# Performance work log

Measured on AMD Instinct MI355X. Metric: run time of the kernel, lower is better.

## Reference

```python
import jax, jax.numpy as jnp
import numpy as np
import math

N, DM, DK, DV, KWIN = 500, 2048, 2048, 2048, 10

def _xavier(key, shape):
    fan_out, fan_in = shape[0], shape[1]
    limit = math.sqrt(6.0 / (fan_in + fan_out))
    return jax.random.uniform(key, (shape[0], shape[1]), jnp.float32, -limit, limit)

def setup_inputs() -> dict:
    key = jax.random.key(0)
    ks = jax.random.split(key, 7)
    X = jax.random.normal(ks[0], (N, DM), jnp.float32)
    mask = jax.random.randint(ks[1], (N, N), 0, 2, jnp.int32)
    # torch Linear weight is (out, in); store transposed so fwd is X @ W
    Wq = _xavier(ks[2], (DK, DM)).T  # [DM, DK]
    Wk = _xavier(ks[3], (DK, DM)).T
    Wv = _xavier(ks[4], (DV, DM)).T
    Wo = _xavier(ks[5], (DM, DV)).T  # [DV, DM]
    wk = _xavier(ks[6], (2 * KWIN + 1, DM))  # relative-position embedding table
    return {"X": X, "mask": mask, "Wq": Wq, "Wk": Wk, "Wv": Wv, "Wo": Wo, "wk": wk}

def reference(X, mask, Wq, Wk, Wv, Wo, wk):
    n = X.shape[0]
    scale = 1.0 / math.sqrt(DK)
    Q = X @ Wq            # [n, dk]
    K = X @ Wk            # [n, dk]
    V = X @ Wv            # [n, dv]
    Qs = Q * scale
    S = Qs @ K.T          # [n, n] content scores
    # relative-position bias: Sr[i,j] = Qs[i] . wk[clip(j-i,-k,k)+k]
    # (Shaw-style gather; identical math to wk[table] matmul, no [n,n,dm] intermediate)
    idx = jnp.clip(jnp.arange(n)[None, :] - jnp.arange(n)[:, None], -KWIN, KWIN) + KWIN  # [n, n]
    QR = Qs @ wk.T                                   # [n, 2k+1]
    Sr = jnp.take_along_axis(QR, idx, axis=1)        # [n, n]
    S = S + Sr
    S = jnp.where(mask == 0, jnp.float32(-1e9), S)
    A = jax.nn.softmax(S, axis=-1)                   # dropout_rate=0 -> identity
    Y = (A @ V) @ Wo                                 # [n, dm]
    return (Y, A)
```

## Files before the change

### kernel.cpp

```cpp
#include <hip/hip_runtime.h>
#include <hip/hip_bf16.h>


#define N_TOK 500
#define MP 512
#define DM 2048
#define KWIN_ 10
#define NREL 21

typedef __hip_bfloat16 bf16;
typedef __attribute__((ext_vector_type(8))) short short8;
typedef __attribute__((ext_vector_type(4))) float floatx4;

#define NS 262144L

__device__ inline float bfj(const short8& v, int j) {
  return __bfloat162float(((const bf16*)&v)[j]);
}

__device__ __forceinline__ void transpose_tile(const float* __restrict__ W,
                                               bf16* __restrict__ Out, int k0,
                                               int n0) {
  __shared__ float t[64][68];
  int tid = threadIdx.x;
  int rr = tid >> 4, cc = (tid & 15) * 4;
  int gsw = cc >> 2;
#pragma unroll
  for (int p = 0; p < 4; ++p) {
    int r = rr + 16 * p;
    float4 v = *(const float4*)(W + (long)(k0 + r) * DM + n0 + cc);
    *(float4*)&t[r][(gsw ^ (r & 3)) * 4] = v;
  }
  __syncthreads();
#pragma unroll
  for (int s0 = 0; s0 < 2; ++s0) {
    int s = tid + s0 * 256;
    int n = s >> 3, c = s & 7;
    bf16 v[8];
#pragma unroll
    for (int j = 0; j < 8; ++j) {
      int rowt = c * 8 + j;
      int col = ((n >> 2) ^ (rowt & 3)) * 4 + (n & 3);
      v[j] = __float2bfloat16(t[rowt][col]);
    }
    *(short8*)(Out + (long)(n0 + n) * DM + k0 + c * 8) = *(short8*)v;
  }
}

__global__ __launch_bounds__(256) void prep(
    const float* __restrict__ Wq, const float* __restrict__ Wk,
    const float* __restrict__ Wv, const float* __restrict__ X,
    const float* __restrict__ wk, bf16* __restrict__ WqkT,
    bf16* __restrict__ WvT, bf16* __restrict__ Xb, bf16* __restrict__ wkb) {
  int z = blockIdx.z;
  int tid = threadIdx.x;
  if (z == 3) {
    int row = blockIdx.y * 32 + blockIdx.x;
    int c0 = tid * 8;
    bf16 v[8];
    if (row < MP) {
      if (row < N_TOK) {
        const float* p = X + (long)row * DM + c0;
#pragma unroll
        for (int j = 0; j < 8; ++j) v[j] = __float2bfloat16(p[j]);
      } else {
#pragma unroll
        for (int j = 0; j < 8; ++j) v[j] = __float2bfloat16(0.f);
      }
      *(short8*)(Xb + (long)row * DM + c0) = *(short8*)v;
    } else if (row < MP + NREL) {
      int r = row - MP;
      const float* p = wk + (long)r * DM + c0;
#pragma unroll
      for (int j = 0; j < 8; ++j) v[j] = __float2bfloat16(p[j]);
      *(short8*)(wkb + (long)r * DM + c0) = *(short8*)v;
    }
    return;
  }
  const float* W = (z == 0) ? Wq : (z == 1) ? Wk : Wv;
  bf16* Out = (z == 0) ? WqkT : (z == 1) ? (WqkT + (long)DM * DM) : WvT;
  transpose_tile(W, Out, blockIdx.y * 64, blockIdx.x * 64);
}

template <int OUT>
__device__ __forceinline__ void gemm_core(
    const bf16* __restrict__ A, int lda, const bf16* __restrict__ B, int ldb,
    float* __restrict__ Cf, bf16* __restrict__ Cb, int ldc, int kStart,
    int kLen, int row0, int col0, int m_store) {
  __shared__ __align__(16) bf16 As[128][32];
  __shared__ __align__(16) bf16 Bs[128][32];
  int tid = threadIdx.x;
  int lane = tid & 63, w = tid >> 6;
  int wr = (w & 1) * 64, wc = (w >> 1) * 64;
  int l16 = lane & 15, l4 = lane >> 4;
  int r1 = tid >> 2, c1 = (tid & 3) * 8;
  const bf16* Ab = A + (long)row0 * lda + kStart;
  const bf16* Bb = B + (long)col0 * ldb + kStart;
  const bf16* a1p = Ab + (long)r1 * lda + c1;
  const bf16* a2p = Ab + (long)(r1 + 64) * lda + c1;
  const bf16* b1p = Bb + (long)r1 * ldb + c1;
  const bf16* b2p = Bb + (long)(r1 + 64) * ldb + c1;
  floatx4 acc[4][4] = {};
  short8 pa0 = *(const short8*)a1p, pa1 = *(const short8*)a2p;
  short8 pb0 = *(const short8*)b1p, pb1 = *(const short8*)b2p;
  for (int k0 = 0; k0 < kLen; k0 += 32) {
    if (k0) __syncthreads();
    *(short8*)&As[r1][c1] = pa0;
    *(short8*)&As[r1 + 64][c1] = pa1;
    *(short8*)&Bs[r1][c1] = pb0;
    *(short8*)&Bs[r1 + 64][c1] = pb1;
    __syncthreads();
    int kn = k0 + 32;
    if (kn < kLen) {
      pa0 = *(const short8*)(a1p + kn);
      pa1 = *(const short8*)(a2p + kn);
      pb0 = *(const short8*)(b1p + kn);
      pb1 = *(const short8*)(b2p + kn);
    }
    short8 af[4], bg[4];
#pragma unroll
    for (int g = 0; g < 4; ++g)
      af[g] = *(short8*)&As[wr + g * 16 + l16][l4 * 8];
#pragma unroll
    for (int g = 0; g < 4; ++g)
      bg[g] = *(short8*)&Bs[wc + g * 16 + l16][l4 * 8];
#pragma unroll
    for (int g = 0; g < 4; ++g)
#pragma unroll
      for (int h = 0; h < 4; ++h)
        acc[g][h] =
            __builtin_amdgcn_mfma_f32_16x16x32_bf16(af[g], bg[h], acc[g][h], 0, 0, 0);
  }
#pragma unroll
  for (int g = 0; g < 4; ++g)
#pragma unroll
    for (int h = 0; h < 4; ++h)
#pragma unroll
      for (int i = 0; i < 4; ++i) {
        long r = row0 + wr + g * 16 + l4 * 4 + i;
        long c = col0 + wc + h * 16 + l16;
        if (OUT == 0)
          Cf[r * ldc + c] = acc[g][h][i];
        else if (OUT == 1)
          Cb[r * ldc + c] = __float2bfloat16(acc[g][h][i]);
        else {
          if (r < m_store) atomicAdd(&Cf[r * ldc + c], acc[g][h][i]);
        }
      }
}

__global__ __launch_bounds__(256, 2) void gemm_qkvt(
    const bf16* __restrict__ Xb, const bf16* __restrict__ WqkT,
    const bf16* __restrict__ WvT, bf16* __restrict__ QKbf,
    bf16* __restrict__ Vtb) {
  int id = blockIdx.x;
  if (id < 128) {
    int col0 = (id & 31) * 128, row0 = (id >> 5) * 128;
    gemm_core<1>(Xb, DM, WqkT, DM, nullptr, QKbf, 4096, 0, DM, row0, col0, 0);
  } else {
    int t = id - 128;
    int col0 = (t & 3) * 128, row0 = (t >> 2) * 128;
    gemm_core<1>(WvT, DM, Xb, DM, nullptr, Vtb, MP, 0, DM, row0, col0, 0);
  }
}

__global__ __launch_bounds__(256, 2) void gemm_s(const bf16* __restrict__ QKbf,
                                                 float* __restrict__ Sp) {
  gemm_core<0>(QKbf, 4096, QKbf + 2048, 4096, Sp + (long)blockIdx.z * NS,
               nullptr, MP, blockIdx.z * 512, 512, blockIdx.y * 128,
               blockIdx.x * 128, 0);
}

__global__ __launch_bounds__(256, 2) void gemm_av_wot(
    const bf16* __restrict__ Abf, const bf16* __restrict__ Vtb,
    bf16* __restrict__ AVbf, const float* __restrict__ Wo,
    bf16* __restrict__ WoT) {
  int id = blockIdx.x;
  if (id < 64) {
    int col0 = (id & 15) * 128, row0 = (id >> 4) * 128;
    gemm_core<1>(Abf, MP, Vtb, MP, nullptr, AVbf, DM, 0, MP, row0, col0, 0);
  } else {
    int t = id - 64;
    transpose_tile(Wo, WoT, (t >> 5) * 64, (t & 31) * 64);
  }
}

__global__ __launch_bounds__(256, 2) void gemm_y(const bf16* __restrict__ AVbf,
                                                 const bf16* __restrict__ WoT,
                                                 float* __restrict__ Yout) {
  gemm_core<2>(AVbf, DM, WoT, DM, Yout, nullptr, DM, blockIdx.z * 1024, 1024,
               blockIdx.y * 128, blockIdx.x * 128, N_TOK);
}

__global__ __launch_bounds__(256) void softmax_qr(
    const float* __restrict__ Sp, const bf16* __restrict__ QKbf,
    const bf16* __restrict__ wkb, const int* __restrict__ mask,
    float* __restrict__ Aout, bf16* __restrict__ Abf,
    float* __restrict__ Yout) {
  int i = blockIdx.x;
  int tid = threadIdx.x;
  if (i >= N_TOK) {
    Abf[(long)i * MP + tid] = __float2bfloat16(0.f);
    Abf[(long)i * MP + tid + 256] = __float2bfloat16(0.f);
    return;
  }
  {
    float4 z4 = {0.f, 0.f, 0.f, 0.f};
    float* yr = Yout + (long)i * DM + tid * 8;
    *(float4*)yr = z4;
    *(float4*)(yr + 4) = z4;
  }
  int lane = tid & 63, w = tid >> 6;
  __shared__ float sQR[24];
  __shared__ float red[4];
  short8 q[4];
#pragma unroll
  for (int s = 0; s < 4; ++s)
    q[s] = *(const short8*)(QKbf + (long)i * 4096 + s * 512 + lane * 8);
  for (int r = w; r < NREL; r += 4) {
    float p = 0.f;
#pragma unroll
    for (int s = 0; s < 4; ++s) {
      short8 wv = *(const short8*)(wkb + (long)r * DM + s * 512 + lane * 8);
#pragma unroll
      for (int j = 0; j < 8; ++j) p += bfj(q[s], j) * bfj(wv, j);
    }
#pragma unroll
    for (int o = 32; o > 0; o >>= 1) p += __shfl_down(p, o);
    if (lane == 0) sQR[r] = p;
  }
  __syncthreads();
  const float scale = 0.022097086912079608f;
  float v0, v1 = -1e30f;
  int j0 = tid, j1 = tid + 256;
  {
    float s = Sp[(long)i * MP + j0] + Sp[NS + (long)i * MP + j0] +
              Sp[2 * NS + (long)i * MP + j0] + Sp[3 * NS + (long)i * MP + j0];
    int rel = j0 - i;
    rel = rel < -KWIN_ ? -KWIN_ : (rel > KWIN_ ? KWIN_ : rel);
    s = scale * (s + sQR[rel + KWIN_]);
    if (mask[(long)i * N_TOK + j0] == 0) s = -1e9f;
    v0 = s;
  }
  if (j1 < N_TOK) {
    float s = Sp[(long)i * MP + j1] + Sp[NS + (long)i * MP + j1] +
              Sp[2 * NS + (long)i * MP + j1] + Sp[3 * NS + (long)i * MP + j1];
    int rel = j1 - i;
    rel = rel < -KWIN_ ? -KWIN_ : (rel > KWIN_ ? KWIN_ : rel);
    s = scale * (s + sQR[rel + KWIN_]);
    if (mask[(long)i * N_TOK + j1] == 0) s = -1e9f;
    v1 = s;
  }
  float mx = fmaxf(v0, v1);
#pragma unroll
  for (int o = 32; o > 0; o >>= 1) mx = fmaxf(mx, __shfl_down(mx, o));
  if (lane == 0) red[w] = mx;
  __syncthreads();
  if (tid == 0) red[0] = fmaxf(fmaxf(red[0], red[1]), fmaxf(red[2], red[3]));
  __syncthreads();
  mx = red[0];
  __syncthreads();
  float e0 = expf(v0 - mx);
  float e1 = (j1 < N_TOK) ? expf(v1 - mx) : 0.f;
  float sum = e0 + e1;
#pragma unroll
  for (int o = 32; o > 0; o >>= 1) sum += __shfl_down(sum, o);
  if (lane == 0) red[w] = sum;
  __syncthreads();
  if (tid == 0) red[0] = red[0] + red[1] + red[2] + red[3];
  __syncthreads();
  float inv = 1.f / red[0];
  float a0 = e0 * inv, a1 = e1 * inv;
  Aout[(long)i * N_TOK + j0] = a0;
  if (j1 < N_TOK) Aout[(long)i * N_TOK + j1] = a1;
  Abf[(long)i * MP + j0] = __float2bfloat16(a0);
  Abf[(long)i * MP + j1] = __float2bfloat16(a1);
}

extern "C" void kernel_launch(void* const* d_in, const int* in_sizes, int n_in,
                              void* d_out, int out_size, void* d_ws,
                              size_t ws_size, hipStream_t stream) {
  const float* X = (const float*)d_in[0];
  const int* mask = (const int*)d_in[1];
  const float* Wq = (const float*)d_in[2];
  const float* Wk = (const float*)d_in[3];
  const float* Wv = (const float*)d_in[4];
  const float* Wo = (const float*)d_in[5];
  const float* wk = (const float*)d_in[6];

  float* Yout = (float*)d_out;
  float* Aout = Yout + (long)N_TOK * DM;

  const long MB = 1 << 20;
  char* p = (char*)d_ws;
  bf16* Xb = (bf16*)p;
  bf16* WqkT = (bf16*)(p + 2 * MB);
  bf16* WvT = (bf16*)(p + 18 * MB);
  bf16* WoT = (bf16*)(p + 26 * MB);
  bf16* wkb = (bf16*)(p + 34 * MB);
  bf16* QKbf = (bf16*)(p + 35 * MB);
  bf16* Vtb = (bf16*)(p + 39 * MB);
  float* Sp = (float*)(p + 41 * MB);
  bf16* Abf = (bf16*)(p + 45 * MB);
  bf16* AVbf = (bf16*)(p + 46 * MB);

  dim3 b256(256);

  prep<<<dim3(32, 32, 4), b256, 0, stream>>>(Wq, Wk, Wv, X, wk, WqkT, WvT, Xb,
                                             wkb);
  gemm_qkvt<<<dim3(192), b256, 0, stream>>>(Xb, WqkT, WvT, QKbf, Vtb);
  gemm_s<<<dim3(4, 4, 4), b256, 0, stream>>>(QKbf, Sp);
  softmax_qr<<<dim3(MP), b256, 0, stream>>>(Sp, QKbf, wkb, mask, Aout, Abf,
                                            Yout);
  gemm_av_wot<<<dim3(1088), b256, 0, stream>>>(Abf, Vtb, AVbf, Wo, WoT);
  gemm_y<<<dim3(16, 4, 2), b256, 0, stream>>>(AVbf, WoT, Yout);
}
```

Baseline: 196.8 us.

## Fuse all stages into one persistent kernel with software grid barriers

Replaces the six separate kernel launches with a single persistent kernel of 256 blocks that runs every stage and separates them with an atomic-counter grid barrier. It also computes Q, K and V in one GEMM and transposes V afterwards, splits the S GEMM into eight K-slices instead of four, and double-buffers the GEMM shared-memory tiles. The aim is to remove launch gaps and raise parallelism. In exchange, the grid barriers require all 256 blocks to be co-resident, and several phases leave most blocks idle.

```diff
diff --git a/kernel.cpp b/kernel.cpp
--- a/kernel.cpp
+++ b/kernel.cpp
@@ -7,6 +7,7 @@
 #define DM 2048
 #define KWIN_ 10
 #define NREL 21
+#define NB 256
 
 typedef __hip_bfloat16 bf16;
 typedef __attribute__((ext_vector_type(8))) short short8;
@@ -18,10 +19,23 @@
   return __bfloat162float(((const bf16*)&v)[j]);
 }
 
+__device__ __forceinline__ void gsync(int* bar, int it) {
+  __syncthreads();
+  if (threadIdx.x == 0) {
+    __threadfence();
+    atomicAdd(bar, 1);
+    while (__hip_atomic_load(bar, __ATOMIC_ACQUIRE,
+                             __HIP_MEMORY_SCOPE_AGENT) < NB * it)
+      __builtin_amdgcn_s_sleep(1);
+  }
+  __syncthreads();
+  __threadfence();
+}
+
 __device__ __forceinline__ void transpose_tile(const float* __restrict__ W,
                                                bf16* __restrict__ Out, int k0,
-                                               int n0) {
-  __shared__ float t[64][68];
+                                               int n0, char* sm) {
+  float (*t)[68] = (float(*)[68])sm;
   int tid = threadIdx.x;
   int rr = tid >> 4, cc = (tid & 15) * 4;
   int gsw = cc >> 2;
@@ -45,91 +59,93 @@
     }
     *(short8*)(Out + (long)(n0 + n) * DM + k0 + c * 8) = *(short8*)v;
   }
-}
-
-__global__ __launch_bounds__(256) void prep(
-    const float* __restrict__ Wq, const float* __restrict__ Wk,
-    const float* __restrict__ Wv, const float* __restrict__ X,
-    const float* __restrict__ wk, bf16* __restrict__ WqkT,
-    bf16* __restrict__ WvT, bf16* __restrict__ Xb, bf16* __restrict__ wkb) {
-  int z = blockIdx.z;
-  int tid = threadIdx.x;
-  if (z == 3) {
-    int row = blockIdx.y * 32 + blockIdx.x;
-    int c0 = tid * 8;
-    bf16 v[8];
-    if (row < MP) {
-      if (row < N_TOK) {
-        const float* p = X + (long)row * DM + c0;
-#pragma unroll
-        for (int j = 0; j < 8; ++j) v[j] = __float2bfloat16(p[j]);
-      } else {
-#pragma unroll
-        for (int j = 0; j < 8; ++j) v[j] = __float2bfloat16(0.f);
-      }
-      *(short8*)(Xb + (long)row * DM + c0) = *(short8*)v;
-    } else if (row < MP + NREL) {
-      int r = row - MP;
-      const float* p = wk + (long)r * DM + c0;
-#pragma unroll
-      for (int j = 0; j < 8; ++j) v[j] = __float2bfloat16(p[j]);
-      *(short8*)(wkb + (long)r * DM + c0) = *(short8*)v;
-    }
-    return;
-  }
-  const float* W = (z == 0) ? Wq : (z == 1) ? Wk : Wv;
-  bf16* Out = (z == 0) ? WqkT : (z == 1) ? (WqkT + (long)DM * DM) : WvT;
-  transpose_tile(W, Out, blockIdx.y * 64, blockIdx.x * 64);
+  __syncthreads();
+}
+
+__device__ __forceinline__ void transpose_bf(const bf16* __restrict__ src,
+                                             int lds, bf16* __restrict__ dst,
+                                             int ldd, int r0, int c0,
+                                             char* sm) {
+  unsigned short (*t)[72] = (unsigned short(*)[72])sm;
+  const unsigned short* s = (const unsigned short*)src;
+  unsigned short* d = (unsigned short*)dst;
+  int tid = threadIdx.x;
+  int c = tid & 63, r4 = tid >> 6;
+#pragma unroll
+  for (int i = 0; i < 16; ++i) {
+    int r = r4 * 16 + i;
+    t[r][c] = s[(long)(r0 + r) * lds + c0 + c];
+  }
+  __syncthreads();
+#pragma unroll
+  for (int i = 0; i < 16; ++i) {
+    int r = r4 * 16 + i;
+    d[(long)(c0 + r) * ldd + r0 + c] = t[c][r];
+  }
+  __syncthreads();
 }
 
 template <int OUT>
 __device__ __forceinline__ void gemm_core(
     const bf16* __restrict__ A, int lda, const bf16* __restrict__ B, int ldb,
     float* __restrict__ Cf, bf16* __restrict__ Cb, int ldc, int kStart,
-    int kLen, int row0, int col0, int m_store) {
-  __shared__ __align__(16) bf16 As[128][32];
-  __shared__ __align__(16) bf16 Bs[128][32];
+    int kLen, int row0, int col0, int m_store, char* sm) {
+  bf16* As = (bf16*)sm;
+  bf16* Bs = (bf16*)(sm + 16384);
   int tid = threadIdx.x;
   int lane = tid & 63, w = tid >> 6;
   int wr = (w & 1) * 64, wc = (w >> 1) * 64;
   int l16 = lane & 15, l4 = lane >> 4;
   int r1 = tid >> 2, c1 = (tid & 3) * 8;
-  const bf16* Ab = A + (long)row0 * lda + kStart;
-  const bf16* Bb = B + (long)col0 * ldb + kStart;
-  const bf16* a1p = Ab + (long)r1 * lda + c1;
-  const bf16* a2p = Ab + (long)(r1 + 64) * lda + c1;
-  const bf16* b1p = Bb + (long)r1 * ldb + c1;
-  const bf16* b2p = Bb + (long)(r1 + 64) * ldb + c1;
+  int soff = r1 * 32 + c1;
+  const bf16* a1p = A + (long)(row0 + r1) * lda + kStart + c1;
+  const bf16* a2p = a1p + 64 * (long)lda;
+  const bf16* b1p = B + (long)(col0 + r1) * ldb + kStart + c1;
+  const bf16* b2p = b1p + 64 * (long)ldb;
   floatx4 acc[4][4] = {};
   short8 pa0 = *(const short8*)a1p, pa1 = *(const short8*)a2p;
   short8 pb0 = *(const short8*)b1p, pb1 = *(const short8*)b2p;
+  *(short8*)(As + soff) = pa0;
+  *(short8*)(As + 2048 + soff) = pa1;
+  *(short8*)(Bs + soff) = pb0;
+  *(short8*)(Bs + 2048 + soff) = pb1;
+  if (kLen > 32) {
+    pa0 = *(const short8*)(a1p + 32);
+    pa1 = *(const short8*)(a2p + 32);
+    pb0 = *(const short8*)(b1p + 32);
+    pb1 = *(const short8*)(b2p + 32);
+  }
+  __syncthreads();
+  int cur = 0;
   for (int k0 = 0; k0 < kLen; k0 += 32) {
-    if (k0) __syncthreads();
-    *(short8*)&As[r1][c1] = pa0;
-    *(short8*)&As[r1 + 64][c1] = pa1;
-    *(short8*)&Bs[r1][c1] = pb0;
-    *(short8*)&Bs[r1 + 64][c1] = pb1;
-    __syncthreads();
-    int kn = k0 + 32;
-    if (kn < kLen) {
-      pa0 = *(const short8*)(a1p + kn);
-      pa1 = *(const short8*)(a2p + kn);
-      pb0 = *(const short8*)(b1p + kn);
-      pb1 = *(const short8*)(b2p + kn);
-    }
+    int cb = cur * 4096, nb = (cur ^ 1) * 4096;
     short8 af[4], bg[4];
 #pragma unroll
     for (int g = 0; g < 4; ++g)
-      af[g] = *(short8*)&As[wr + g * 16 + l16][l4 * 8];
+      af[g] = *(short8*)(As + cb + (wr + g * 16 + l16) * 32 + l4 * 8);
 #pragma unroll
     for (int g = 0; g < 4; ++g)
-      bg[g] = *(short8*)&Bs[wc + g * 16 + l16][l4 * 8];
+      bg[g] = *(short8*)(Bs + cb + (wc + g * 16 + l16) * 32 + l4 * 8);
+    if (k0 + 32 < kLen) {
+      *(short8*)(As + nb + soff) = pa0;
+      *(short8*)(As + nb + 2048 + soff) = pa1;
+      *(short8*)(Bs + nb + soff) = pb0;
+      *(short8*)(Bs + nb + 2048 + soff) = pb1;
+      if (k0 + 64 < kLen) {
+        pa0 = *(const short8*)(a1p + k0 + 64);
+        pa1 = *(const short8*)(a2p + k0 + 64);
+        pb0 = *(const short8*)(b1p + k0 + 64);
+        pb1 = *(const short8*)(b2p + k0 + 64);
+      }
+    }
 #pragma unroll
     for (int g = 0; g < 4; ++g)
 #pragma unroll
       for (int h = 0; h < 4; ++h)
         acc[g][h] =
             __builtin_amdgcn_mfma_f32_16x16x32_bf16(af[g], bg[h], acc[g][h], 0, 0, 0);
+    __syncthreads();
+    cur ^= 1;
   }
 #pragma unroll
   for (int g = 0; g < 4; ++g)
@@ -143,80 +159,28 @@
           Cf[r * ldc + c] = acc[g][h][i];
         else if (OUT == 1)
           Cb[r * ldc + c] = __float2bfloat16(acc[g][h][i]);
-        else {
-          if (r < m_store) atomicAdd(&Cf[r * ldc + c], acc[g][h][i]);
-        }
+        else if (r < m_store)
+          atomicAdd(&Cf[r * ldc + c], acc[g][h][i]);
       }
 }
 
-__global__ __launch_bounds__(256, 2) void gemm_qkvt(
-    const bf16* __restrict__ Xb, const bf16* __restrict__ WqkT,
-    const bf16* __restrict__ WvT, bf16* __restrict__ QKbf,
-    bf16* __restrict__ Vtb) {
-  int id = blockIdx.x;
-  if (id < 128) {
-    int col0 = (id & 31) * 128, row0 = (id >> 5) * 128;
-    gemm_core<1>(Xb, DM, WqkT, DM, nullptr, QKbf, 4096, 0, DM, row0, col0, 0);
-  } else {
-    int t = id - 128;
-    int col0 = (t & 3) * 128, row0 = (t >> 2) * 128;
-    gemm_core<1>(WvT, DM, Xb, DM, nullptr, Vtb, MP, 0, DM, row0, col0, 0);
-  }
-}
-
-__global__ __launch_bounds__(256, 2) void gemm_s(const bf16* __restrict__ QKbf,
-                                                 float* __restrict__ Sp) {
-  gemm_core<0>(QKbf, 4096, QKbf + 2048, 4096, Sp + (long)blockIdx.z * NS,
-               nullptr, MP, blockIdx.z * 512, 512, blockIdx.y * 128,
-               blockIdx.x * 128, 0);
-}
-
-__global__ __launch_bounds__(256, 2) void gemm_av_wot(
-    const bf16* __restrict__ Abf, const bf16* __restrict__ Vtb,
-    bf16* __restrict__ AVbf, const float* __restrict__ Wo,
-    bf16* __restrict__ WoT) {
-  int id = blockIdx.x;
-  if (id < 64) {
-    int col0 = (id & 15) * 128, row0 = (id >> 4) * 128;
-    gemm_core<1>(Abf, MP, Vtb, MP, nullptr, AVbf, DM, 0, MP, row0, col0, 0);
-  } else {
-    int t = id - 64;
-    transpose_tile(Wo, WoT, (t >> 5) * 64, (t & 31) * 64);
-  }
-}
-
-__global__ __launch_bounds__(256, 2) void gemm_y(const bf16* __restrict__ AVbf,
-                                                 const bf16* __restrict__ WoT,
-                                                 float* __restrict__ Yout) {
-  gemm_core<2>(AVbf, DM, WoT, DM, Yout, nullptr, DM, blockIdx.z * 1024, 1024,
-               blockIdx.y * 128, blockIdx.x * 128, N_TOK);
-}
-
-__global__ __launch_bounds__(256) void softmax_qr(
-    const float* __restrict__ Sp, const bf16* __restrict__ QKbf,
+__device__ __forceinline__ void softmax_row(
+    int i, const float* __restrict__ Sp, const bf16* __restrict__ QKVbf,
     const bf16* __restrict__ wkb, const int* __restrict__ mask,
-    float* __restrict__ Aout, bf16* __restrict__ Abf,
-    float* __restrict__ Yout) {
-  int i = blockIdx.x;
+    float* __restrict__ Aout, bf16* __restrict__ Abf, char* sm) {
   int tid = threadIdx.x;
   if (i >= N_TOK) {
     Abf[(long)i * MP + tid] = __float2bfloat16(0.f);
     Abf[(long)i * MP + tid + 256] = __float2bfloat16(0.f);
     return;
   }
-  {
-    float4 z4 = {0.f, 0.f, 0.f, 0.f};
-    float* yr = Yout + (long)i * DM + tid * 8;
-    *(float4*)yr = z4;
-    *(float4*)(yr + 4) = z4;
-  }
+  float* sQR = (float*)sm;
+  float* red = (float*)sm + 24;
   int lane = tid & 63, w = tid >> 6;
-  __shared__ float sQR[24];
-  __shared__ float red[4];
   short8 q[4];
 #pragma unroll
   for (int s = 0; s < 4; ++s)
-    q[s] = *(const short8*)(QKbf + (long)i * 4096 + s * 512 + lane * 8);
+    q[s] = *(const short8*)(QKVbf + (long)i * 6144 + s * 512 + lane * 8);
   for (int r = w; r < NREL; r += 4) {
     float p = 0.f;
 #pragma unroll
@@ -234,8 +198,9 @@
   float v0, v1 = -1e30f;
   int j0 = tid, j1 = tid + 256;
   {
-    float s = Sp[(long)i * MP + j0] + Sp[NS + (long)i * MP + j0] +
-              Sp[2 * NS + (long)i * MP + j0] + Sp[3 * NS + (long)i * MP + j0];
+    float s = 0.f;
+#pragma unroll
+    for (int z = 0; z < 8; ++z) s += Sp[z * NS + (long)i * MP + j0];
     int rel = j0 - i;
     rel = rel < -KWIN_ ? -KWIN_ : (rel > KWIN_ ? KWIN_ : rel);
     s = scale * (s + sQR[rel + KWIN_]);
@@ -243,8 +208,9 @@
     v0 = s;
   }
   if (j1 < N_TOK) {
-    float s = Sp[(long)i * MP + j1] + Sp[NS + (long)i * MP + j1] +
-              Sp[2 * NS + (long)i * MP + j1] + Sp[3 * NS + (long)i * MP + j1];
+    float s = 0.f;
+#pragma unroll
+    for (int z = 0; z < 8; ++z) s += Sp[z * NS + (long)i * MP + j1];
     int rel = j1 - i;
     rel = rel < -KWIN_ ? -KWIN_ : (rel > KWIN_ ? KWIN_ : rel);
     s = scale * (s + sQR[rel + KWIN_]);
@@ -275,6 +241,102 @@
   if (j1 < N_TOK) Aout[(long)i * N_TOK + j1] = a1;
   Abf[(long)i * MP + j0] = __float2bfloat16(a0);
   Abf[(long)i * MP + j1] = __float2bfloat16(a1);
+  __syncthreads();
+}
+
+__global__ __launch_bounds__(256, 1) void fused(
+    const float* __restrict__ X, const int* __restrict__ mask,
+    const float* __restrict__ Wq, const float* __restrict__ Wk,
+    const float* __restrict__ Wv, const float* __restrict__ Wo,
+    const float* __restrict__ wk, float* __restrict__ Yout,
+    float* __restrict__ Aout, char* __restrict__ ws, int* __restrict__ bar) {
+  __shared__ __align__(16) char sm[32768];
+  const long MB = 1 << 20;
+  bf16* Xb = (bf16*)ws;
+  bf16* WqkvT = (bf16*)(ws + 2 * MB);
+  bf16* WoT = (bf16*)(ws + 26 * MB);
+  bf16* wkb = (bf16*)(ws + 34 * MB);
+  bf16* QKVbf = (bf16*)(ws + 35 * MB);
+  bf16* Vtb = (bf16*)(ws + 41 * MB);
+  float* Sp = (float*)(ws + 43 * MB);
+  bf16* Abf = (bf16*)(ws + 51 * MB);
+  bf16* AVbf = (bf16*)(ws + 52 * MB);
+  int bid = blockIdx.x;
+  int tid = threadIdx.x;
+
+  for (int j = bid; j < 4105; j += NB) {
+    if (j < 3072) {
+      int z = j >> 10, t = j & 1023;
+      const float* W = (z == 0) ? Wq : (z == 1) ? Wk : Wv;
+      transpose_tile(W, WqkvT + (long)z * DM * DM, (t >> 5) * 64,
+                     (t & 31) * 64, sm);
+    } else if (j < 3605) {
+      int r = j - 3072;
+      bf16 v[8];
+      if (r < MP) {
+        if (r < N_TOK) {
+          const float* p = X + (long)r * DM + tid * 8;
+#pragma unroll
+          for (int q = 0; q < 8; ++q) v[q] = __float2bfloat16(p[q]);
+        } else {
+#pragma unroll
+          for (int q = 0; q < 8; ++q) v[q] = __float2bfloat16(0.f);
+        }
+        *(short8*)(Xb + (long)r * DM + tid * 8) = *(short8*)v;
+      } else {
+        int rr = r - MP;
+        const float* p = wk + (long)rr * DM + tid * 8;
+#pragma unroll
+        for (int q = 0; q < 8; ++q) v[q] = __float2bfloat16(p[q]);
+        *(short8*)(wkb + (long)rr * DM + tid * 8) = *(short8*)v;
+      }
+    } else {
+      int r = j - 3605;
+      float4 z4 = {0.f, 0.f, 0.f, 0.f};
+      float* yr = Yout + (long)r * DM + tid * 8;
+      *(float4*)yr = z4;
+      *(float4*)(yr + 4) = z4;
+    }
+  }
+  gsync(bar, 1);
+
+  if (bid < 192) {
+    int row0 = (bid / 48) * 128, col0 = (bid % 48) * 128;
+    gemm_core<1>(Xb, DM, WqkvT, DM, nullptr, QKVbf, 6144, 0, DM, row0, col0,
+                 0, sm);
+  } else {
+    for (int t = bid - 192; t < 1024; t += 64)
+      transpose_tile(Wo, WoT, (t >> 5) * 64, (t & 31) * 64, sm);
+  }
+  gsync(bar, 2);
+
+  for (int j = bid; j < 384; j += NB) {
+    if (j < 128) {
+      int z = j >> 4, t = j & 15;
+      gemm_core<0>(QKVbf, 6144, QKVbf + 2048, 6144, Sp + (long)z * NS, nullptr,
+                   MP, z * 256, 256, (t >> 2) * 128, (t & 3) * 128, 0, sm);
+    } else {
+      int t = j - 128;
+      transpose_bf(QKVbf + 4096, 6144, Vtb, MP, (t >> 5) * 64, (t & 31) * 64,
+                   sm);
+    }
+  }
+  gsync(bar, 3);
+
+  for (int i = bid; i < MP; i += NB)
+    softmax_row(i, Sp, QKVbf, wkb, mask, Aout, Abf, sm);
+  gsync(bar, 4);
+
+  if (bid < 64)
+    gemm_core<1>(Abf, MP, Vtb, MP, nullptr, AVbf, DM, 0, MP, (bid >> 4) * 128,
+                 (bid & 15) * 128, 0, sm);
+  gsync(bar, 5);
+
+  if (bid < 128) {
+    int z = bid >> 6, t = bid & 63;
+    gemm_core<2>(AVbf, DM, WoT, DM, Yout, nullptr, DM, z * 1024, 1024,
+                 (t >> 4) * 128, (t & 15) * 128, N_TOK, sm);
+  }
 }
 
 extern "C" void kernel_launch(void* const* d_in, const int* in_sizes, int n_in,
@@ -291,27 +353,10 @@
   float* Yout = (float*)d_out;
   float* Aout = Yout + (long)N_TOK * DM;
 
-  const long MB = 1 << 20;
-  char* p = (char*)d_ws;
-  bf16* Xb = (bf16*)p;
-  bf16* WqkT = (bf16*)(p + 2 * MB);
-  bf16* WvT = (bf16*)(p + 18 * MB);
-  bf16* WoT = (bf16*)(p + 26 * MB);
-  bf16* wkb = (bf16*)(p + 34 * MB);
-  bf16* QKbf = (bf16*)(p + 35 * MB);
-  bf16* Vtb = (bf16*)(p + 39 * MB);
-  float* Sp = (float*)(p + 41 * MB);
-  bf16* Abf = (bf16*)(p + 45 * MB);
-  bf16* AVbf = (bf16*)(p + 46 * MB);
-
-  dim3 b256(256);
-
-  prep<<<dim3(32, 32, 4), b256, 0, stream>>>(Wq, Wk, Wv, X, wk, WqkT, WvT, Xb,
-                                             wkb);
-  gemm_qkvt<<<dim3(192), b256, 0, stream>>>(Xb, WqkT, WvT, QKbf, Vtb);
-  gemm_s<<<dim3(4, 4, 4), b256, 0, stream>>>(QKbf, Sp);
-  softmax_qr<<<dim3(MP), b256, 0, stream>>>(Sp, QKbf, wkb, mask, Aout, Abf,
-                                            Yout);
-  gemm_av_wot<<<dim3(1088), b256, 0, stream>>>(Abf, Vtb, AVbf, Wo, WoT);
-  gemm_y<<<dim3(16, 4, 2), b256, 0, stream>>>(AVbf, WoT, Yout);
-}
+  char* ws = (char*)d_ws;
+  int* bar = (int*)(ws + 56 * (1L << 20));
+
+  hipMemsetAsync(bar, 0, 256, stream);
+  fused<<<dim3(NB), dim3(256), 0, stream>>>(X, mask, Wq, Wk, Wv, Wo, wk, Yout,
+                                            Aout, ws, bar);
+}
```

After: 427.1 us. 2.17x slower.
